# Kernel tuning notes

Measured on AMD Instinct MI355X. Metric: run time of the kernel, lower is better.

The kernel has to match this reference:

```python
import jax, jax.numpy as jnp
import numpy as np

B, T, H, V, S = 32, 1024, 512, 1024, 128
PAD = 0          # PAD_token, also the CTC blank
NEG = -1e30      # finite stand-in for -inf (grad-safe)


def setup_inputs() -> dict:
    key = jax.random.key(0)
    ks = jax.random.split(key, 5)
    padded_input = jax.random.normal(ks[0], (B, T, H), dtype=jnp.float32)
    # labels in [1, V) so no PAD inside targets -> target_lengths == S
    padded_target = jax.random.randint(ks[1], (B, S), 1, V).astype(jnp.int32)
    input_lengths = jax.random.randint(ks[2], (B,), T // 2, T + 1).astype(jnp.int32)
    W1 = jax.random.normal(ks[3], (H, H), dtype=jnp.float32) * 0.02
    b1 = jnp.zeros((H,), jnp.float32)
    W2 = jax.random.normal(ks[4], (H, V), dtype=jnp.float32) * 0.02
    b2 = jnp.zeros((V,), jnp.float32)
    return {"padded_target": padded_target, "padded_input": padded_input,
            "input_lengths": input_lengths, "W1": W1, "b1": b1, "W2": W2, "b2": b2}


def _ctc_loss(log_probs, targets, input_lengths, target_lengths, blank=PAD):
    """CTC negative log-likelihood per example (reduction='none').
    log_probs: [B,T,V] (log-softmaxed), targets: [B,S] int."""
    Bb, Tt, _ = log_probs.shape
    Ss = targets.shape[1]
    L = 2 * Ss + 1  # extended label sequence: blank,y1,blank,...,yS,blank
    ext = jnp.full((Bb, L), blank, dtype=targets.dtype).at[:, 1::2].set(targets)
    # gather log-probs of extended labels: [B,T,L] -> [T,B,L]
    lp_ext = jnp.take_along_axis(
        log_probs, jnp.broadcast_to(ext[:, None, :], (Bb, Tt, L)), axis=2)
    lp_ext = jnp.transpose(lp_ext, (1, 0, 2))
    # skip transition (s-2 -> s) allowed when ext[s] != blank and ext[s] != ext[s-2]
    skip = jnp.concatenate(
        [jnp.zeros((Bb, 2), bool),
         (ext[:, 2:] != blank) & (ext[:, 2:] != ext[:, :-2])], axis=1)

    alpha0 = jnp.full((Bb, L), NEG, jnp.float32)
    alpha0 = alpha0.at[:, 0].set(lp_ext[0, :, 0]).at[:, 1].set(lp_ext[0, :, 1])

    def step(alpha, xs):
        lp_t, t = xs
        s1 = jnp.concatenate([jnp.full((Bb, 1), NEG, jnp.float32), alpha[:, :-1]], axis=1)
        s2 = jnp.concatenate([jnp.full((Bb, 2), NEG, jnp.float32), alpha[:, :-2]], axis=1)
        a = jnp.logaddexp(alpha, s1)
        a = jnp.where(skip, jnp.logaddexp(a, s2), a)
        new = a + lp_t
        # freeze alpha past each example's input length
        new = jnp.where((t < input_lengths)[:, None], new, alpha)
        return new, None

    alpha, _ = jax.lax.scan(step, alpha0, (lp_ext[1:], jnp.arange(1, Tt)))
    end1 = jnp.take_along_axis(alpha, (2 * target_lengths - 1)[:, None], axis=1)[:, 0]
    end2 = jnp.take_along_axis(alpha, (2 * target_lengths)[:, None], axis=1)[:, 0]
    return -jnp.logaddexp(end1, end2)


def reference(padded_target, padded_input, input_lengths, W1, b1, W2, b2):
    target_lengths = jnp.sum(padded_target != PAD, axis=1).astype(jnp.int32)
    h = jnp.tanh(padded_input @ W1 + b1)          # [B,T,H]
    logits = h @ W2 + b2                           # [B,T,V]
    log_probs = jax.nn.log_softmax(logits, axis=-1)
    loss = _ctc_loss(log_probs, padded_target, input_lengths, target_lengths)
    return loss / target_lengths.astype(jnp.float32)  # [B]
```

## Files before the change

kernel.cpp:

```cpp
#include <hip/hip_runtime.h>
#include <hip/hip_bf16.h>
#include <math.h>

#define Bq 32
#define Tt 1024
#define Hh 512
#define Vv 1024
#define Ss 128

typedef short bf16x8 __attribute__((ext_vector_type(8)));
typedef float f32x4 __attribute__((ext_vector_type(4)));

#define GLDS(srcp, dstp, sz) \
  __builtin_amdgcn_global_load_lds( \
      (const __attribute__((address_space(1))) void*)(srcp), \
      (__attribute__((address_space(3))) void*)(dstp), sz, 0, 0)

__device__ __forceinline__ ushort f2bf(float v) {
  __hip_bfloat16 hv = __float2bfloat16(v);
  return *(ushort*)&hv;
}

template <int N>
__device__ __forceinline__ void wb() {
  __asm__ volatile("s_waitcnt vmcnt(%0)" ::"i"(N) : "memory");
  __builtin_amdgcn_s_barrier();
}

#define BFLY_ADD(v) { \
  v += __int_as_float(__builtin_amdgcn_ds_swizzle(__float_as_int(v), 0x041F)); \
  v += __int_as_float(__builtin_amdgcn_ds_swizzle(__float_as_int(v), 0x081F)); \
  v += __int_as_float(__builtin_amdgcn_ds_swizzle(__float_as_int(v), 0x101F)); \
  v += __int_as_float(__builtin_amdgcn_ds_swizzle(__float_as_int(v), 0x201F)); }

__global__ void transpose_cvt(const float* __restrict__ in, ushort* __restrict__ out,
                              int K, int N) {
  __shared__ float tile[32][33];
  const int k0 = blockIdx.y * 32, n0 = blockIdx.x * 32;
  const int tx = threadIdx.x, ty = threadIdx.y;
  for (int i = ty; i < 32; i += 8)
    tile[i][tx] = in[(size_t)(k0 + i) * N + n0 + tx];
  __syncthreads();
  for (int i = ty; i < 32; i += 8)
    out[(size_t)(n0 + i) * K + k0 + tx] = f2bf(tile[tx][i]);
}

__global__ __launch_bounds__(256, 2)
void gemm1_fused(const float* __restrict__ X, const ushort* __restrict__ Bt,
                 const float* __restrict__ bias, const int* __restrict__ lens,
                 ushort* __restrict__ H) {
  __shared__ ushort Bs[4][128 * 64];
  const int row0 = blockIdx.x * 64;
  if ((row0 & (Tt - 1)) >= lens[blockIdx.x >> 4]) return;

  const int tid = threadIdx.x;
  const int lane = tid & 63, wave = tid >> 6;
  const int wm = wave >> 1, wn = wave & 1;
  const int q = lane >> 4, r16 = lane & 15;
  const int lrow = lane >> 3;
  const int swz = (lane & 7) ^ lrow;
  const int rx = r16 & 7;
  const int kx0 = (q ^ rx) * 8;
  const int kx1 = ((4 + q) ^ rx) * 8;

  float bcolAll[4][4];
#pragma unroll
  for (int nt = 0; nt < 4; ++nt)
#pragma unroll
    for (int ni = 0; ni < 4; ++ni)
      bcolAll[nt][ni] = bias[nt * 128 + wn * 64 + ni * 16 + r16];

  bf16x8 af[16][2];
#pragma unroll
  for (int ks = 0; ks < 16; ++ks)
#pragma unroll
    for (int mi = 0; mi < 2; ++mi) {
      const float* src = X + (size_t)(row0 + wm * 32 + mi * 16 + r16) * Hh + ks * 32 + q * 8;
      const float4 f0 = *(const float4*)(src);
      const float4 f1 = *(const float4*)(src + 4);
      union { bf16x8 v; ushort u[8]; } pk;
      pk.u[0] = f2bf(f0.x); pk.u[1] = f2bf(f0.y); pk.u[2] = f2bf(f0.z); pk.u[3] = f2bf(f0.w);
      pk.u[4] = f2bf(f1.x); pk.u[5] = f2bf(f1.y); pk.u[6] = f2bf(f1.z); pk.u[7] = f2bf(f1.w);
      af[ks][mi] = pk.v;
    }

  auto stageF = [&](int nt2, int kc2, int d2) {
#pragma unroll
    for (int i = 0; i < 4; ++i) {
      const int seg = wave * 4 + i;
      const int rr = seg * 8 + lrow;
      GLDS(Bt + (size_t)(nt2 * 128 + rr) * Hh + kc2 * 64 + swz * 8, &Bs[d2][seg * 512], 16);
    }
  };

  stageF(0, 0, 0);
  stageF(0, 1, 1);

  f32x4 acc[2][4];
#pragma unroll
  for (int i = 0; i < 2; ++i)
#pragma unroll
    for (int j = 0; j < 4; ++j) acc[i][j] = (f32x4){0.f, 0.f, 0.f, 0.f};

  for (int nt = 0; nt < 4; ++nt) {
#pragma unroll
    for (int kc = 0; kc < 8; ++kc) {
      if (nt < 3 || kc < 7) wb<4>(); else wb<0>();
      if (nt < 3 || kc < 6)
        stageF(nt + (kc >= 6 ? 1 : 0), (kc + 2) & 7, (kc + 2) & 3);
      const int d = kc & 3;
#pragma unroll
      for (int ksl = 0; ksl < 2; ++ksl) {
        const int kxo = ksl ? kx1 : kx0;
        bf16x8 bfr[4];
#pragma unroll
        for (int ni = 0; ni < 4; ++ni)
          bfr[ni] = *(const bf16x8*)(&Bs[d][((wn * 64 + ni * 16 + r16) << 6) + kxo]);
#pragma unroll
        for (int mi = 0; mi < 2; ++mi)
#pragma unroll
          for (int ni = 0; ni < 4; ++ni)
            acc[mi][ni] = __builtin_amdgcn_mfma_f32_16x16x32_bf16(af[kc * 2 + ksl][mi], bfr[ni], acc[mi][ni], 0, 0, 0);
      }
    }
#pragma unroll
    for (int mi = 0; mi < 2; ++mi)
#pragma unroll
      for (int r = 0; r < 4; ++r) {
        const int row = row0 + wm * 32 + mi * 16 + q * 4 + r;
#pragma unroll
        for (int ni = 0; ni < 4; ++ni) {
          const float v = acc[mi][ni][r] + bcolAll[nt][ni];
          const float ex = __expf(2.0f * v);
          const float th = (ex - 1.0f) / (ex + 1.0f);
          H[(size_t)row * Hh + nt * 128 + wn * 64 + ni * 16 + r16] = f2bf(th);
        }
        acc[mi][0][r] = 0.f; acc[mi][1][r] = 0.f; acc[mi][2][r] = 0.f; acc[mi][3][r] = 0.f;
      }
  }
}

__global__ __launch_bounds__(256, 2)
void gemm2sm(const ushort* __restrict__ Aq, const ushort* __restrict__ Bt,
             const float* __restrict__ bias, const int* __restrict__ tgt,
             const int* __restrict__ lens,
             ushort* __restrict__ pOdd, ushort* __restrict__ pBlank) {
  __shared__ ushort Bs[4][128 * 64];
  __shared__ float biasLds[Vv];
  __shared__ int tgLds[128];
  __shared__ float blankL[64];
  __shared__ float rowSum[64];
  __shared__ float tmpP[2][64];

  const int row0 = blockIdx.x * 64;
  const int bEx = blockIdx.x >> 4;
  if ((row0 & (Tt - 1)) >= lens[bEx]) return;

  const int tid = threadIdx.x;
  const int lane = tid & 63, wave = tid >> 6;
  const int wm = wave >> 1, wn = wave & 1;
  const int q = lane >> 4, r16 = lane & 15;
  const int lrow = lane >> 3;
  const int swz = (lane & 7) ^ lrow;
  const int rx = r16 & 7;
  const int kx0 = (q ^ rx) * 8;
  const int kx1 = ((4 + q) ^ rx) * 8;

  GLDS(bias + tid * 4, (char*)biasLds + wave * 1024, 16);
  if (tid < 128) tgLds[tid] = tgt[bEx * Ss + tid];

  bf16x8 af[16][2];
#pragma unroll
  for (int ks = 0; ks < 16; ++ks)
#pragma unroll
    for (int mi = 0; mi < 2; ++mi)
      af[ks][mi] = *(const bf16x8*)(Aq + (size_t)(row0 + wm * 32 + mi * 16 + r16) * Hh + ks * 32 + q * 8);

  auto stageF = [&](int nt2, int kc2, int d2) {
#pragma unroll
    for (int i = 0; i < 4; ++i) {
      const int seg = wave * 4 + i;
      const int rr = seg * 8 + lrow;
      const ushort* src = (nt2 < 8)
          ? Bt + (size_t)(nt2 * 128 + rr) * Hh + kc2 * 64 + swz * 8
          : Bt + (size_t)tgLds[rr] * Hh + kc2 * 64 + swz * 8;
      GLDS(src, &Bs[d2][seg * 512], 16);
    }
  };

  stageF(0, 0, 0);
  stageF(0, 1, 1);
  __asm__ volatile("s_waitcnt lgkmcnt(0)" ::: "memory");

  f32x4 acc[2][4];
#pragma unroll
  for (int i = 0; i < 2; ++i)
#pragma unroll
    for (int j = 0; j < 4; ++j) acc[i][j] = (f32x4){0.f, 0.f, 0.f, 0.f};
  float rowP[2][4] = {{0.f, 0.f, 0.f, 0.f}, {0.f, 0.f, 0.f, 0.f}};

  for (int nt = 0; nt < 9; ++nt) {
#pragma unroll
    for (int kc = 0; kc < 8; ++kc) {
      if (nt < 8 || kc < 7) wb<4>(); else wb<0>();
      if (nt < 8 || kc < 6)
        stageF(nt + (kc >= 6 ? 1 : 0), (kc + 2) & 7, (kc + 2) & 3);
      const int d = kc & 3;
#pragma unroll
      for (int ksl = 0; ksl < 2; ++ksl) {
        const int kxo = ksl ? kx1 : kx0;
        bf16x8 bfr[4];
#pragma unroll
        for (int ni = 0; ni < 4; ++ni)
          bfr[ni] = *(const bf16x8*)(&Bs[d][((wn * 64 + ni * 16 + r16) << 6) + kxo]);
#pragma unroll
        for (int mi = 0; mi < 2; ++mi)
#pragma unroll
          for (int ni = 0; ni < 4; ++ni)
            acc[mi][ni] = __builtin_amdgcn_mfma_f32_16x16x32_bf16(af[kc * 2 + ksl][mi], bfr[ni], acc[mi][ni], 0, 0, 0);
      }
    }

    if (nt < 8) {
      float bcol[4];
#pragma unroll
      for (int ni = 0; ni < 4; ++ni) bcol[ni] = biasLds[nt * 128 + wn * 64 + ni * 16 + r16];
      if (nt == 0 && wn == 0 && r16 == 0) {
#pragma unroll
        for (int mi = 0; mi < 2; ++mi)
#pragma unroll
          for (int r = 0; r < 4; ++r)
            blankL[wm * 32 + mi * 16 + q * 4 + r] = acc[mi][0][r] + bcol[0];
      }
#pragma unroll
      for (int mi = 0; mi < 2; ++mi)
#pragma unroll
        for (int r = 0; r < 4; ++r) {
          float s = __expf(acc[mi][0][r] + bcol[0]);
          s += __expf(acc[mi][1][r] + bcol[1]);
          s += __expf(acc[mi][2][r] + bcol[2]);
          s += __expf(acc[mi][3][r] + bcol[3]);
          rowP[mi][r] += s;
          acc[mi][0][r] = 0.f; acc[mi][1][r] = 0.f; acc[mi][2][r] = 0.f; acc[mi][3][r] = 0.f;
        }
      if (nt == 7) {
        float sred[2][4];
#pragma unroll
        for (int mi = 0; mi < 2; ++mi)
#pragma unroll
          for (int r = 0; r < 4; ++r) {
            float s = rowP[mi][r];
            BFLY_ADD(s);
            sred[mi][r] = s;
          }
        if (r16 == 0) {
#pragma unroll
          for (int mi = 0; mi < 2; ++mi) {
            float4 w = {sred[mi][0], sred[mi][1], sred[mi][2], sred[mi][3]};
            *(float4*)&tmpP[wn][wm * 32 + mi * 16 + q * 4] = w;
          }
        }
        __syncthreads();
        if (tid < 64) {
          const float tot = tmpP[0][tid] + tmpP[1][tid];
          rowSum[tid] = tot;
          pBlank[row0 + tid] = f2bf(__expf(blankL[tid]) * 64.0f / tot);
        }
        __syncthreads();
      }
    } else {
      float bcl[4];
#pragma unroll
      for (int ni = 0; ni < 4; ++ni) bcl[ni] = biasLds[tgLds[wn * 64 + ni * 16 + r16]];
#pragma unroll
      for (int mi = 0; mi < 2; ++mi) {
        const float4 rs4 = *(const float4*)&rowSum[wm * 32 + mi * 16 + q * 4];
#pragma unroll
        for (int r = 0; r < 4; ++r) {
          const float sc = 64.0f / ((const float*)&rs4)[r];
          const int row = row0 + wm * 32 + mi * 16 + q * 4 + r;
#pragma unroll
          for (int ni = 0; ni < 4; ++ni) {
            const float p = __expf(acc[mi][ni][r] + bcl[ni]) * sc;
            pOdd[(size_t)row * Ss + wn * 64 + ni * 16 + r16] = f2bf(p);
          }
        }
      }
    }
  }
}

__device__ __forceinline__ float dpp_wshr1(float x) {
  return __int_as_float(__builtin_amdgcn_update_dpp(
      0, __float_as_int(x), 0x138, 0xf, 0xf, true));
}
__device__ __forceinline__ float dpp_wave_max(float m) {
  m = fmaxf(m, __int_as_float(__builtin_amdgcn_update_dpp(0, __float_as_int(m), 0x111, 0xf, 0xf, true)));
  m = fmaxf(m, __int_as_float(__builtin_amdgcn_update_dpp(0, __float_as_int(m), 0x112, 0xf, 0xf, true)));
  m = fmaxf(m, __int_as_float(__builtin_amdgcn_update_dpp(0, __float_as_int(m), 0x114, 0xf, 0xf, true)));
  m = fmaxf(m, __int_as_float(__builtin_amdgcn_update_dpp(0, __float_as_int(m), 0x118, 0xf, 0xf, true)));
  m = fmaxf(m, __int_as_float(__builtin_amdgcn_update_dpp(__float_as_int(m), __float_as_int(m), 0x142, 0xf, 0xf, false)));
  m = fmaxf(m, __int_as_float(__builtin_amdgcn_update_dpp(__float_as_int(m), __float_as_int(m), 0x143, 0xf, 0xf, false)));
  return __int_as_float(__builtin_amdgcn_readlane(__float_as_int(m), 63));
}

__global__ __launch_bounds__(64)
void ctc_dp(const ushort* __restrict__ pOddG, const ushort* __restrict__ pBlankG,
            const int* __restrict__ tgt, const int* __restrict__ lens,
            float* __restrict__ out) {
  __shared__ ushort pO[2][72 * 128];
  __shared__ ushort pBl[2][128];
  const int b = blockIdx.x, l = threadIdx.x;
  const ushort* pObase = pOddG + (size_t)b * Tt * Ss;
  const ushort* pBbase = pBlankG + (size_t)b * Tt;
  const int* tg = tgt + b * Ss;
  const int len = lens[b];

  float sk1 = 0.f, sk3;
  if (l >= 1) sk1 = (tg[2 * l] != tg[2 * l - 1]) ? 1.f : 0.f;
  sk3 = (tg[2 * l + 1] != tg[2 * l]) ? 1.f : 0.f;

  auto stage = [&](int c, int d) {
    const ushort* src = pObase + (size_t)c * 64 * 128;
#pragma unroll
    for (int i = 0; i < 16; ++i)
      GLDS(src + (i * 64 + l) * 8, &pO[d][i * 512], 16);
    GLDS(pBbase + c * 64 + l * 2, &pBl[d][0], 4);
  };

  stage(0, 0);
  __syncthreads();

  float a0 = 0.f, a1 = 0.f, a2 = 0.f, a3 = 0.f, a4 = 0.f;
  if (l == 0) {
    a0 = __int_as_float(((unsigned)pBl[0][0]) << 16);
    a1 = __int_as_float(((unsigned)pO[0][0]) << 16);
  }
  int E = 0;

  auto renorm = [&]() {
    float m = fmaxf(fmaxf(fmaxf(a0, a1), fmaxf(a2, a3)), a4);
    const float gm = dpp_wave_max(m);
    const int e = (int)((__float_as_uint(gm) >> 23) & 255) - 127;
    int sh = 30 - e; if (sh > 120) sh = 120;
    const float scale = __uint_as_float((unsigned)(127 + sh) << 23);
    E -= sh;
    a0 *= scale; a1 *= scale; a2 *= scale; a3 *= scale; a4 *= scale;
  };

  auto run_dyn = [&](int d, int stA, int stB, int tbase) {
    const int n = stB - stA;
    if (n <= 0) return;
    unsigned qL[4], qB[4];
#pragma unroll
    for (int k = 0; k < 4; ++k) {
      const int st = stA + k;
      qL[k] = *(const unsigned*)&pO[d][(st << 7) + 2 * l];
      qB[k] = (unsigned)pBl[d][st];
    }
    auto body = [&](int i, int k) {
      const float pOa = __int_as_float(qL[k] << 16);
      const float pObv = __int_as_float(qL[k] & 0xffff0000u);
      const float pB = __int_as_float(qB[k] << 16);
      const float h3 = dpp_wshr1(a3);
      const float n0 = (a0 + h3) * pB;
      const float n1 = fmaf(sk1, h3, a1 + a0) * pOa;
      const float n2 = (a2 + a1) * pB;
      const float n3 = fmaf(sk3, a1, a3 + a2) * pObv;
      const float n4 = (a4 + a3) * pB;
      a0 = n0; a1 = n1; a2 = n2; a3 = n3; a4 = n4;
      const int st2 = stA + i + 4;
      qL[k] = *(const unsigned*)&pO[d][(st2 << 7) + 2 * l];
      qB[k] = (unsigned)pBl[d][st2];
      if (((tbase + i) & 7) == 0) renorm();
    };
    int i = 0;
    for (; i + 4 <= n; i += 4) { body(i, 0); body(i + 1, 1); body(i + 2, 2); body(i + 3, 3); }
    if ((n & 3) > 0) body(i, 0);
    if ((n & 3) > 1) body(i + 1, 1);
    if ((n & 3) > 2) body(i + 2, 2);
  };

  auto run_full = [&](int d) {
    unsigned qL[8], qB[4];
#pragma unroll
    for (int k = 0; k < 8; ++k)
      qL[k] = *(const unsigned*)&pO[d][(k << 7) + 2 * l];
#pragma unroll
    for (int j = 0; j < 4; ++j)
      qB[j] = *(const unsigned*)&pBl[d][2 * j];
    for (int i = 0; i < 64; i += 8) {
#pragma unroll
      for (int k = 0; k < 8; ++k) {
        const float pOa = __int_as_float(qL[k] << 16);
        const float pObv = __int_as_float(qL[k] & 0xffff0000u);
        const unsigned bb = qB[k >> 1];
        const float pB = __int_as_float((k & 1) ? (bb & 0xffff0000u) : (bb << 16));
        const float h3 = dpp_wshr1(a3);
        const float n0 = (a0 + h3) * pB;
        const float n1 = fmaf(sk1, h3, a1 + a0) * pOa;
        const float n2 = (a2 + a1) * pB;
        const float n3 = fmaf(sk3, a1, a3 + a2) * pObv;
        const float n4 = (a4 + a3) * pB;
        a0 = n0; a1 = n1; a2 = n2; a3 = n3; a4 = n4;
        qL[k] = *(const unsigned*)&pO[d][((i + k + 8) << 7) + 2 * l];
        if (k & 1) qB[k >> 1] = *(const unsigned*)&pBl[d][i + k + 7];
        if (k == 0) renorm();
      }
    }
  };

  if (64 < len) stage(1, 1);
  run_dyn(0, 1, (64 < len) ? 64 : len, 1);
  __syncthreads();
  const int Cfull = len >> 6;
  for (int c = 1; c < Cfull; ++c) {
    const int d = c & 1;
    if ((c + 1) * 64 < len) stage(c + 1, d ^ 1);
    run_full(d);
    __syncthreads();
  }
  if (len & 63) run_dyn(Cfull & 1, 0, len & 63, Cfull * 64);

  const int tl = __popcll(__ballot(tg[l] != 0)) + __popcll(__ballot(tg[64 + l] != 0));
  const int s1 = 2 * tl - 1, s2 = 2 * tl;
  float v = 0.f;
  const int sb = 4 * l;
  if (sb == s1 || sb == s2) v += a0;
  if (sb + 1 == s1 || sb + 1 == s2) v += a1;
  if (sb + 2 == s1 || sb + 2 == s2) v += a2;
  if (sb + 3 == s1 || sb + 3 == s2) v += a3;
  if (l == 63 && s2 == 256) v += a4;
#pragma unroll
  for (int off = 1; off < 64; off <<= 1) v += __shfl_xor(v, off);
  if (l == 0)
    out[b] = -((log2f(v) + (float)E - 6.0f * (float)len) * 0.6931471805599453f) / (float)tl;
}

extern "C" void kernel_launch(void* const* d_in, const int* in_sizes, int n_in,
                              void* d_out, int out_size, void* d_ws, size_t ws_size,
                              hipStream_t stream) {
  const int*   targets = (const int*)d_in[0];
  const float* X       = (const float*)d_in[1];
  const int*   lens    = (const int*)d_in[2];
  const float* W1      = (const float*)d_in[3];
  const float* b1      = (const float*)d_in[4];
  const float* W2      = (const float*)d_in[5];
  const float* b2      = (const float*)d_in[6];
  float* out = (float*)d_out;

  ushort* h       = (ushort*)d_ws;
  ushort* W1T     = h + (size_t)Bq * Tt * Hh;
  ushort* W2T     = W1T + (size_t)Hh * Hh;
  ushort* pOddG   = W2T + (size_t)Vv * Hh;
  ushort* pBlankG = pOddG + (size_t)Bq * Tt * Ss;

  transpose_cvt<<<dim3(Hh / 32, Hh / 32), dim3(32, 8), 0, stream>>>(W1, W1T, Hh, Hh);
  transpose_cvt<<<dim3(Vv / 32, Hh / 32), dim3(32, 8), 0, stream>>>(W2, W2T, Hh, Vv);
  gemm1_fused<<<dim3((Bq * Tt) / 64), dim3(256), 0, stream>>>(X, W1T, b1, lens, h);
  gemm2sm<<<dim3((Bq * Tt) / 64), dim3(256), 0, stream>>>(h, W2T, b2, targets, lens, pOddG, pBlankG);
  ctc_dp<<<dim3(Bq), dim3(64), 0, stream>>>(pOddG, pBlankG, targets, lens, out);
}
```

Baseline: 237.0 us.

## Double-buffer LDS B-fragments in GEMMs and merge weight transposes into one launch

Both GEMM kernels now read the next k-chunk's B fragments from LDS into registers (bnxt) while the MFMAs for the current chunk use bcur. This hides LDS read latency behind matrix math, and the wait/stage order is rearranged to match. The epilogues move inside the k loop at kc==7. The two weight-transpose launches become one 768-block kernel, and the A-fragment loads in gemm2 are issued before the bias/target setup. In exchange, register pressure rises from the extra fragment buffers, which could hurt occupancy under launch_bounds(256,2).

```diff
diff --git a/kernel.cpp b/kernel.cpp
--- a/kernel.cpp
+++ b/kernel.cpp
@@ -33,10 +33,14 @@
   v += __int_as_float(__builtin_amdgcn_ds_swizzle(__float_as_int(v), 0x101F)); \
   v += __int_as_float(__builtin_amdgcn_ds_swizzle(__float_as_int(v), 0x201F)); }
 
-__global__ void transpose_cvt(const float* __restrict__ in, ushort* __restrict__ out,
-                              int K, int N) {
+__global__ void transpose_cvt2(const float* __restrict__ W1, const float* __restrict__ W2,
+                               ushort* __restrict__ W1T, ushort* __restrict__ W2T) {
   __shared__ float tile[32][33];
-  const int k0 = blockIdx.y * 32, n0 = blockIdx.x * 32;
+  const int bid = blockIdx.x;
+  const float* in; ushort* out; int K, N, bx, by;
+  if (bid < 256) { in = W1; out = W1T; K = Hh; N = Hh; bx = bid & 15; by = bid >> 4; }
+  else { const int b2 = bid - 256; in = W2; out = W2T; K = Hh; N = Vv; bx = b2 & 31; by = b2 >> 5; }
+  const int k0 = by * 32, n0 = bx * 32;
   const int tx = threadIdx.x, ty = threadIdx.y;
   for (int i = ty; i < 32; i += 8)
     tile[i][tx] = in[(size_t)(k0 + i) * N + n0 + tx];
@@ -92,9 +96,19 @@
       GLDS(Bt + (size_t)(nt2 * 128 + rr) * Hh + kc2 * 64 + swz * 8, &Bs[d2][seg * 512], 16);
     }
   };
+  auto readFrags = [&](bf16x8 (&bfr)[2][4], int d) {
+#pragma unroll
+    for (int ni = 0; ni < 4; ++ni) {
+      bfr[0][ni] = *(const bf16x8*)(&Bs[d][((wn * 64 + ni * 16 + r16) << 6) + kx0]);
+      bfr[1][ni] = *(const bf16x8*)(&Bs[d][((wn * 64 + ni * 16 + r16) << 6) + kx1]);
+    }
+  };
 
   stageF(0, 0, 0);
   stageF(0, 1, 1);
+  wb<4>();
+  bf16x8 bcur[2][4], bnxt[2][4];
+  readFrags(bcur, 0);
 
   f32x4 acc[2][4];
 #pragma unroll
@@ -105,38 +119,41 @@
   for (int nt = 0; nt < 4; ++nt) {
 #pragma unroll
     for (int kc = 0; kc < 8; ++kc) {
-      if (nt < 3 || kc < 7) wb<4>(); else wb<0>();
-      if (nt < 3 || kc < 6)
-        stageF(nt + (kc >= 6 ? 1 : 0), (kc + 2) & 7, (kc + 2) & 3);
-      const int d = kc & 3;
-#pragma unroll
-      for (int ksl = 0; ksl < 2; ++ksl) {
-        const int kxo = ksl ? kx1 : kx0;
-        bf16x8 bfr[4];
-#pragma unroll
-        for (int ni = 0; ni < 4; ++ni)
-          bfr[ni] = *(const bf16x8*)(&Bs[d][((wn * 64 + ni * 16 + r16) << 6) + kxo]);
+      const bool haveS = !(nt == 3 && kc >= 6);
+      const bool haveN = !(nt == 3 && kc == 7);
+      if (haveS) stageF(nt + (kc >= 6 ? 1 : 0), (kc + 2) & 7, (kc + 2) & 3);
+      if (haveN) {
+        if (haveS) wb<4>(); else wb<0>();
+        readFrags(bnxt, (kc + 1) & 3);
+      }
+#pragma unroll
+      for (int ksl = 0; ksl < 2; ++ksl)
 #pragma unroll
         for (int mi = 0; mi < 2; ++mi)
 #pragma unroll
           for (int ni = 0; ni < 4; ++ni)
-            acc[mi][ni] = __builtin_amdgcn_mfma_f32_16x16x32_bf16(af[kc * 2 + ksl][mi], bfr[ni], acc[mi][ni], 0, 0, 0);
+            acc[mi][ni] = __builtin_amdgcn_mfma_f32_16x16x32_bf16(af[kc * 2 + ksl][mi], bcur[ksl][ni], acc[mi][ni], 0, 0, 0);
+#pragma unroll
+      for (int z = 0; z < 2; ++z)
+#pragma unroll
+        for (int ni = 0; ni < 4; ++ni) bcur[z][ni] = bnxt[z][ni];
+      if (kc == 7) {
+#pragma unroll
+        for (int mi = 0; mi < 2; ++mi)
+#pragma unroll
+          for (int r = 0; r < 4; ++r) {
+            const int row = row0 + wm * 32 + mi * 16 + q * 4 + r;
+#pragma unroll
+            for (int ni = 0; ni < 4; ++ni) {
+              const float v = acc[mi][ni][r] + bcolAll[nt][ni];
+              const float ex = __expf(2.0f * v);
+              const float th = (ex - 1.0f) / (ex + 1.0f);
+              H[(size_t)row * Hh + nt * 128 + wn * 64 + ni * 16 + r16] = f2bf(th);
+            }
+            acc[mi][0][r] = 0.f; acc[mi][1][r] = 0.f; acc[mi][2][r] = 0.f; acc[mi][3][r] = 0.f;
+          }
       }
     }
-#pragma unroll
-    for (int mi = 0; mi < 2; ++mi)
-#pragma unroll
-      for (int r = 0; r < 4; ++r) {
-        const int row = row0 + wm * 32 + mi * 16 + q * 4 + r;
-#pragma unroll
-        for (int ni = 0; ni < 4; ++ni) {
-          const float v = acc[mi][ni][r] + bcolAll[nt][ni];
-          const float ex = __expf(2.0f * v);
-          const float th = (ex - 1.0f) / (ex + 1.0f);
-          H[(size_t)row * Hh + nt * 128 + wn * 64 + ni * 16 + r16] = f2bf(th);
-        }
-        acc[mi][0][r] = 0.f; acc[mi][1][r] = 0.f; acc[mi][2][r] = 0.f; acc[mi][3][r] = 0.f;
-      }
   }
 }
 
@@ -166,15 +183,15 @@
   const int kx0 = (q ^ rx) * 8;
   const int kx1 = ((4 + q) ^ rx) * 8;
 
+  bf16x8 af[16][2];
+#pragma unroll
+  for (int ks = 0; ks < 16; ++ks)
+#pragma unroll
+    for (int mi = 0; mi < 2; ++mi)
+      af[ks][mi] = *(const bf16x8*)(Aq + (size_t)(row0 + wm * 32 + mi * 16 + r16) * Hh + ks * 32 + q * 8);
+
   GLDS(bias + tid * 4, (char*)biasLds + wave * 1024, 16);
   if (tid < 128) tgLds[tid] = tgt[bEx * Ss + tid];
-
-  bf16x8 af[16][2];
-#pragma unroll
-  for (int ks = 0; ks < 16; ++ks)
-#pragma unroll
-    for (int mi = 0; mi < 2; ++mi)
-      af[ks][mi] = *(const bf16x8*)(Aq + (size_t)(row0 + wm * 32 + mi * 16 + r16) * Hh + ks * 32 + q * 8);
 
   auto stageF = [&](int nt2, int kc2, int d2) {
 #pragma unroll
@@ -187,10 +204,20 @@
       GLDS(src, &Bs[d2][seg * 512], 16);
     }
   };
+  auto readFrags = [&](bf16x8 (&bfr)[2][4], int d) {
+#pragma unroll
+    for (int ni = 0; ni < 4; ++ni) {
+      bfr[0][ni] = *(const bf16x8*)(&Bs[d][((wn * 64 + ni * 16 + r16) << 6) + kx0]);
+      bfr[1][ni] = *(const bf16x8*)(&Bs[d][((wn * 64 + ni * 16 + r16) << 6) + kx1]);
+    }
+  };
 
   stageF(0, 0, 0);
   stageF(0, 1, 1);
   __asm__ volatile("s_waitcnt lgkmcnt(0)" ::: "memory");
+  wb<4>();
+  bf16x8 bcur[2][4], bnxt[2][4];
+  readFrags(bcur, 0);
 
   f32x4 acc[2][4];
 #pragma unroll
@@ -202,87 +229,90 @@
   for (int nt = 0; nt < 9; ++nt) {
 #pragma unroll
     for (int kc = 0; kc < 8; ++kc) {
-      if (nt < 8 || kc < 7) wb<4>(); else wb<0>();
-      if (nt < 8 || kc < 6)
-        stageF(nt + (kc >= 6 ? 1 : 0), (kc + 2) & 7, (kc + 2) & 3);
-      const int d = kc & 3;
-#pragma unroll
-      for (int ksl = 0; ksl < 2; ++ksl) {
-        const int kxo = ksl ? kx1 : kx0;
-        bf16x8 bfr[4];
-#pragma unroll
-        for (int ni = 0; ni < 4; ++ni)
-          bfr[ni] = *(const bf16x8*)(&Bs[d][((wn * 64 + ni * 16 + r16) << 6) + kxo]);
+      const bool haveS = !(nt == 8 && kc >= 6);
+      const bool haveN = !(nt == 8 && kc == 7);
+      if (haveS) stageF(nt + (kc >= 6 ? 1 : 0), (kc + 2) & 7, (kc + 2) & 3);
+      if (haveN) {
+        if (haveS) wb<4>(); else wb<0>();
+        readFrags(bnxt, (kc + 1) & 3);
+      }
+#pragma unroll
+      for (int ksl = 0; ksl < 2; ++ksl)
 #pragma unroll
         for (int mi = 0; mi < 2; ++mi)
 #pragma unroll
           for (int ni = 0; ni < 4; ++ni)
-            acc[mi][ni] = __builtin_amdgcn_mfma_f32_16x16x32_bf16(af[kc * 2 + ksl][mi], bfr[ni], acc[mi][ni], 0, 0, 0);
-      }
-    }
-
-    if (nt < 8) {
-      float bcol[4];
-#pragma unroll
-      for (int ni = 0; ni < 4; ++ni) bcol[ni] = biasLds[nt * 128 + wn * 64 + ni * 16 + r16];
-      if (nt == 0 && wn == 0 && r16 == 0) {
-#pragma unroll
-        for (int mi = 0; mi < 2; ++mi)
-#pragma unroll
-          for (int r = 0; r < 4; ++r)
-            blankL[wm * 32 + mi * 16 + q * 4 + r] = acc[mi][0][r] + bcol[0];
-      }
-#pragma unroll
-      for (int mi = 0; mi < 2; ++mi)
-#pragma unroll
-        for (int r = 0; r < 4; ++r) {
-          float s = __expf(acc[mi][0][r] + bcol[0]);
-          s += __expf(acc[mi][1][r] + bcol[1]);
-          s += __expf(acc[mi][2][r] + bcol[2]);
-          s += __expf(acc[mi][3][r] + bcol[3]);
-          rowP[mi][r] += s;
-          acc[mi][0][r] = 0.f; acc[mi][1][r] = 0.f; acc[mi][2][r] = 0.f; acc[mi][3][r] = 0.f;
-        }
-      if (nt == 7) {
-        float sred[2][4];
-#pragma unroll
-        for (int mi = 0; mi < 2; ++mi)
-#pragma unroll
-          for (int r = 0; r < 4; ++r) {
-            float s = rowP[mi][r];
-            BFLY_ADD(s);
-            sred[mi][r] = s;
+            acc[mi][ni] = __builtin_amdgcn_mfma_f32_16x16x32_bf16(af[kc * 2 + ksl][mi], bcur[ksl][ni], acc[mi][ni], 0, 0, 0);
+#pragma unroll
+      for (int z = 0; z < 2; ++z)
+#pragma unroll
+        for (int ni = 0; ni < 4; ++ni) bcur[z][ni] = bnxt[z][ni];
+
+      if (kc == 7) {
+        if (nt < 8) {
+          float bcol[4];
+#pragma unroll
+          for (int ni = 0; ni < 4; ++ni) bcol[ni] = biasLds[nt * 128 + wn * 64 + ni * 16 + r16];
+          if (nt == 0 && wn == 0 && r16 == 0) {
+#pragma unroll
+            for (int mi = 0; mi < 2; ++mi)
+#pragma unroll
+              for (int r = 0; r < 4; ++r)
+                blankL[wm * 32 + mi * 16 + q * 4 + r] = acc[mi][0][r] + bcol[0];
           }
-        if (r16 == 0) {
+#pragma unroll
+          for (int mi = 0; mi < 2; ++mi)
+#pragma unroll
+            for (int r = 0; r < 4; ++r) {
+              float s = __expf(acc[mi][0][r] + bcol[0]);
+              s += __expf(acc[mi][1][r] + bcol[1]);
+              s += __expf(acc[mi][2][r] + bcol[2]);
+              s += __expf(acc[mi][3][r] + bcol[3]);
+              rowP[mi][r] += s;
+              acc[mi][0][r] = 0.f; acc[mi][1][r] = 0.f; acc[mi][2][r] = 0.f; acc[mi][3][r] = 0.f;
+            }
+          if (nt == 7) {
+            float sred[2][4];
+#pragma unroll
+            for (int mi = 0; mi < 2; ++mi)
+#pragma unroll
+              for (int r = 0; r < 4; ++r) {
+                float s = rowP[mi][r];
+                BFLY_ADD(s);
+                sred[mi][r] = s;
+              }
+            if (r16 == 0) {
+#pragma unroll
+              for (int mi = 0; mi < 2; ++mi) {
+                float4 w = {sred[mi][0], sred[mi][1], sred[mi][2], sred[mi][3]};
+                *(float4*)&tmpP[wn][wm * 32 + mi * 16 + q * 4] = w;
+              }
+            }
+            __syncthreads();
+            if (tid < 64) {
+              const float tot = tmpP[0][tid] + tmpP[1][tid];
+              rowSum[tid] = tot;
+              pBlank[row0 + tid] = f2bf(__expf(blankL[tid]) * 64.0f / tot);
+            }
+            __syncthreads();
+          }
+        } else {
+          float bcl[4];
+#pragma unroll
+          for (int ni = 0; ni < 4; ++ni) bcl[ni] = biasLds[tgLds[wn * 64 + ni * 16 + r16]];
 #pragma unroll
           for (int mi = 0; mi < 2; ++mi) {
-            float4 w = {sred[mi][0], sred[mi][1], sred[mi][2], sred[mi][3]};
-            *(float4*)&tmpP[wn][wm * 32 + mi * 16 + q * 4] = w;
-          }
-        }
-        __syncthreads();
-        if (tid < 64) {
-          const float tot = tmpP[0][tid] + tmpP[1][tid];
-          rowSum[tid] = tot;
-          pBlank[row0 + tid] = f2bf(__expf(blankL[tid]) * 64.0f / tot);
-        }
-        __syncthreads();
-      }
-    } else {
-      float bcl[4];
-#pragma unroll
-      for (int ni = 0; ni < 4; ++ni) bcl[ni] = biasLds[tgLds[wn * 64 + ni * 16 + r16]];
-#pragma unroll
-      for (int mi = 0; mi < 2; ++mi) {
-        const float4 rs4 = *(const float4*)&rowSum[wm * 32 + mi * 16 + q * 4];
-#pragma unroll
-        for (int r = 0; r < 4; ++r) {
-          const float sc = 64.0f / ((const float*)&rs4)[r];
-          const int row = row0 + wm * 32 + mi * 16 + q * 4 + r;
-#pragma unroll
-          for (int ni = 0; ni < 4; ++ni) {
-            const float p = __expf(acc[mi][ni][r] + bcl[ni]) * sc;
-            pOdd[(size_t)row * Ss + wn * 64 + ni * 16 + r16] = f2bf(p);
+            const float4 rs4 = *(const float4*)&rowSum[wm * 32 + mi * 16 + q * 4];
+#pragma unroll
+            for (int r = 0; r < 4; ++r) {
+              const float sc = 64.0f / ((const float*)&rs4)[r];
+              const int row = row0 + wm * 32 + mi * 16 + q * 4 + r;
+#pragma unroll
+              for (int ni = 0; ni < 4; ++ni) {
+                const float p = __expf(acc[mi][ni][r] + bcl[ni]) * sc;
+                pOdd[(size_t)row * Ss + wn * 64 + ni * 16 + r16] = f2bf(p);
+              }
+            }
           }
         }
       }
@@ -455,8 +485,7 @@
   ushort* pOddG   = W2T + (size_t)Vv * Hh;
   ushort* pBlankG = pOddG + (size_t)Bq * Tt * Ss;
 
-  transpose_cvt<<<dim3(Hh / 32, Hh / 32), dim3(32, 8), 0, stream>>>(W1, W1T, Hh, Hh);
-  transpose_cvt<<<dim3(Vv / 32, Hh / 32), dim3(32, 8), 0, stream>>>(W2, W2T, Hh, Vv);
+  transpose_cvt2<<<dim3(768), dim3(32, 8), 0, stream>>>(W1, W2, W1T, W2T);
   gemm1_fused<<<dim3((Bq * Tt) / 64), dim3(256), 0, stream>>>(X, W1T, b1, lens, h);
   gemm2sm<<<dim3((Bq * Tt) / 64), dim3(256), 0, stream>>>(h, W2T, b2, targets, lens, pOddG, pBlankG);
   ctc_dp<<<dim3(Bq), dim3(64), 0, stream>>>(pOddG, pBlankG, targets, lens, out);
```

New measurement: 236.2 us. About the same (-0.3%).
